# Optimization experiments

Measured on AMD Instinct MI355X. Metric: run time of the kernel, lower is better.

The kernel has to match this reference:

```python
import math
import jax, jax.numpy as jnp
import numpy as np

B, T, D = 8, 2048, 1024

def _gelu(x):
    # tanh-approx GELU, matching the torch module's _gelu
    c = math.sqrt(2.0 / math.pi)
    return 0.5 * x * (1.0 + jnp.tanh(c * (x + 0.044715 * x * x * x)))

def _normalize(x, axis):
    # matches F.normalize(eps=1e-12)
    n = jnp.linalg.norm(x, axis=axis, keepdims=True)
    return x / jnp.maximum(n, 1e-12)

def setup_inputs() -> dict:
    key = jax.random.key(0)
    k1, k2 = jax.random.split(key)
    x = jax.random.normal(k1, (B, T, D), dtype=jnp.float32)
    ema_out = _normalize(jax.random.normal(k2, (D,), dtype=jnp.float32), 0)[..., 0] if False else None
    ema = jax.random.normal(k2, (D,), dtype=jnp.float32)
    ema = ema / jnp.maximum(jnp.linalg.norm(ema), 1e-12)
    return {
        "x": x,
        "ema_out": ema,
        "logit_decay": jnp.float32(math.log(0.9 / 0.1)),
        "log_tau": jnp.float32(math.log(2.0)),
        "log_blend": jnp.float32(math.log(0.3 / 0.7)),
        "logit_blend_seq": jnp.float32(0.0),
    }

def reference(x, ema_out, logit_decay, log_tau, log_blend, logit_blend_seq):
    Bx, Tx, Dx = x.shape
    tau = jnp.exp(log_tau)
    alpha = jax.nn.sigmoid(log_blend)
    w_seq = jax.nn.sigmoid(logit_blend_seq)

    out = _gelu(x)                              # [B,T,D]
    out_norm = _normalize(out, -1)              # [B,T,D]
    ema_norm = ema_out / jnp.maximum(jnp.linalg.norm(ema_out), 1e-12)  # [D]

    ema_sim = jnp.einsum('btd,d->bt', out_norm, ema_norm)             # [B,T]
    sim_mat = jnp.einsum('btd,bsd->bts', out_norm, out_norm)          # [B,T,T]

    causal = jnp.tril(jnp.ones((Tx, Tx), dtype=bool), k=-1)           # strict past
    sim_past = jnp.where(causal[None], sim_mat, -2.0)
    seq_sim = jnp.max(sim_past, axis=-1)                              # [B,T]

    has_past = (jnp.arange(Tx) > 0)[None, :]                          # [1,T]
    seq_sim = jnp.where(has_past, seq_sim, ema_sim)

    familiarity = w_seq * seq_sim + (1.0 - w_seq) * ema_sim
    novelty = jnp.exp(-tau * familiarity)
    gate = 1.0 - alpha + alpha * novelty                              # [B,T]
    return out * gate[..., None]
```

## Files before the change

### kernel.cpp

```cpp
#include <hip/hip_runtime.h>
#include <math.h>

#define NB 8
#define TT 2048
#define DD 1024
#define NTI 16
#define NPAIR 136

typedef __attribute__((ext_vector_type(4))) int intx4;
typedef __attribute__((ext_vector_type(4))) float floatx4;

__device__ inline float fast_gelu(float x) {
    float z = 0.7978845608028654f * (x + 0.044715f * x * x * x);
    float e = __expf(2.0f * z);
    float th = 1.0f - 2.0f / (e + 1.0f);
    return 0.5f * x * (1.0f + th);
}

__global__ __launch_bounds__(256) void k_gelu_norm(
        const float* __restrict__ x, const float* __restrict__ ema,
        unsigned int* __restrict__ onrm8, float* __restrict__ ema_sim) {
    int row = blockIdx.x * 4 + (threadIdx.x >> 6);
    int lane = threadIdx.x & 63;
    const float4* xr = reinterpret_cast<const float4*>(x + (size_t)row * DD);
    const float4* er = reinterpret_cast<const float4*>(ema);
    float g[16];
    float ss = 0.f, dt = 0.f, e2 = 0.f;
#pragma unroll
    for (int j = 0; j < 4; ++j) {
        float4 v = xr[j * 64 + lane];
        float4 e = er[j * 64 + lane];
        float vv[4] = {v.x, v.y, v.z, v.w};
        float ee[4] = {e.x, e.y, e.z, e.w};
        e2 += ee[0] * ee[0] + ee[1] * ee[1] + ee[2] * ee[2] + ee[3] * ee[3];
#pragma unroll
        for (int i = 0; i < 4; ++i) {
            float o = fast_gelu(vv[i]);
            g[j * 4 + i] = o;
            ss += o * o;
            dt += o * ee[i];
        }
    }
#pragma unroll
    for (int m = 1; m < 64; m <<= 1) {
        ss += __shfl_xor(ss, m);
        dt += __shfl_xor(dt, m);
        e2 += __shfl_xor(e2, m);
    }
    float inv = 1.0f / fmaxf(sqrtf(ss), 1e-12f);
    float einv = 1.0f / fmaxf(sqrtf(e2), 1e-12f);
    unsigned int* o8 = onrm8 + (size_t)row * (DD / 4);
#pragma unroll
    for (int j = 0; j < 4; ++j) {
        int q0 = (int)rintf(g[j * 4 + 0] * inv * 127.0f);
        int q1 = (int)rintf(g[j * 4 + 1] * inv * 127.0f);
        int q2 = (int)rintf(g[j * 4 + 2] * inv * 127.0f);
        int q3 = (int)rintf(g[j * 4 + 3] * inv * 127.0f);
        unsigned pk = (q0 & 255) | ((q1 & 255) << 8) | ((q2 & 255) << 16) |
                      ((unsigned)(q3 & 255) << 24);
        o8[j * 64 + lane] = pk;
    }
    if (lane == 0) ema_sim[row] = dt * inv * einv;
}

__global__ __launch_bounds__(256) void k_seqmax(const unsigned char* __restrict__ onrm8,
                                                float* __restrict__ part) {
    __shared__ __align__(16) unsigned char lds[32768];

    int id = blockIdx.x;
    int nid = (id & 7) * NPAIR + (id >> 3);
    int b = nid / NPAIR;
    int p = nid % NPAIR;
    int ti = (int)((sqrtf(8.0f * (float)p + 1.0f) - 1.0f) * 0.5f);
    while ((ti + 1) * (ti + 2) / 2 <= p) ++ti;
    while (ti * (ti + 1) / 2 > p) --ti;
    int sj = p - ti * (ti + 1) / 2;

    int lane = threadIdx.x & 63;
    int wave = threadIdx.x >> 6;
    int wr = wave >> 1, wc = wave & 1;
    int rl = lane & 15, g = lane >> 4;

    const unsigned char* Abase = onrm8 + (size_t)(b * TT + ti * 128) * DD;
    const unsigned char* Bbase = onrm8 + (size_t)(b * TT + sj * 128) * DD;

    intx4 acc[4][4];
#pragma unroll
    for (int i = 0; i < 4; i++)
#pragma unroll
        for (int j = 0; j < 4; j++) acc[i][j] = (intx4){0, 0, 0, 0};

    auto stage = [&](int kt) {
#pragma unroll
        for (int i = 0; i < 4; ++i) {
            int c = wave * 4 + i;
            int off = c * 1024 + lane * 16;
            int row = off >> 7;
            int colb = (off & 127) ^ ((row & 7) << 4);
            const unsigned char* srcA = Abase + (size_t)row * DD + kt * 128 + colb;
            const unsigned char* srcB = Bbase + (size_t)row * DD + kt * 128 + colb;
            __builtin_amdgcn_global_load_lds(
                (const __attribute__((address_space(1))) unsigned int*)srcA,
                (__attribute__((address_space(3))) unsigned int*)(&lds[0] + c * 1024),
                16, 0, 0);
            __builtin_amdgcn_global_load_lds(
                (const __attribute__((address_space(1))) unsigned int*)srcB,
                (__attribute__((address_space(3))) unsigned int*)(&lds[16384] + c * 1024),
                16, 0, 0);
        }
    };

    auto ldfrag = [&](const unsigned char* base, int r, int ks) -> intx4 {
        int sw = (r & 7) << 4;
        return *(const intx4*)(base + r * 128 + ((ks * 64 + g * 16) ^ sw));
    };

    for (int kt = 0; kt < 8; ++kt) {
        stage(kt);
        __syncthreads();
#pragma unroll
        for (int ks = 0; ks < 2; ++ks) {
            intx4 af[4], bg[4];
#pragma unroll
            for (int f = 0; f < 4; ++f) {
                af[f] = ldfrag(&lds[0], wr * 64 + f * 16 + rl, ks);
                bg[f] = ldfrag(&lds[16384], wc * 64 + f * 16 + rl, ks);
            }
#pragma unroll
            for (int fi = 0; fi < 4; ++fi)
#pragma unroll
                for (int fj = 0; fj < 4; ++fj)
                    acc[fi][fj] = __builtin_amdgcn_mfma_i32_16x16x64_i8(
                        af[fi], bg[fj], acc[fi][fj], 0, 0, 0);
        }
        __syncthreads();
    }

    const float qs = 1.0f / 16129.0f;
    int t0g = ti * 128 + wr * 64;
    int s0g = sj * 128 + wc * 64;
#pragma unroll
    for (int fi = 0; fi < 4; ++fi) {
#pragma unroll
        for (int r = 0; r < 4; ++r) {
            int trow = t0g + fi * 16 + g * 4 + r;
            float m = -2.0f;
#pragma unroll
            for (int fj = 0; fj < 4; ++fj) {
                int scol = s0g + fj * 16 + rl;
                float v = (float)acc[fi][fj][r] * qs;
                m = fmaxf(m, (scol < trow) ? v : -2.0f);
            }
#pragma unroll
            for (int msk = 1; msk < 16; msk <<= 1) m = fmaxf(m, __shfl_xor(m, msk));
            if (rl == 0)
                part[(((size_t)b * 32 + sj * 2 + wc) << 11) + trow] = m;
        }
    }
}

__global__ __launch_bounds__(256) void k_gate(
        const float* __restrict__ x, float* __restrict__ out,
        const float* __restrict__ ema_sim, const float* __restrict__ part,
        const float* __restrict__ log_tau,
        const float* __restrict__ log_blend,
        const float* __restrict__ logit_blend_seq) {
    int row = blockIdx.x * 4 + (threadIdx.x >> 6);
    int lane = threadIdx.x & 63;
    int b = row >> 11;
    int t = row & (TT - 1);

    int n = 2 * ((t >> 7) + 1);
    float m = (lane < n) ? part[(((size_t)b * 32 + lane) << 11) + t] : -2.0f;
#pragma unroll
    for (int msk = 1; msk < 64; msk <<= 1) m = fmaxf(m, __shfl_xor(m, msk));

    float tau = __expf(log_tau[0]);
    float alpha = 1.f / (1.f + __expf(-log_blend[0]));
    float wseq = 1.f / (1.f + __expf(-logit_blend_seq[0]));
    float es = ema_sim[row];
    float sq = (t > 0) ? m : es;
    float fam = wseq * sq + (1.f - wseq) * es;
    float gate = 1.f - alpha + alpha * __expf(-tau * fam);

    const float4* xr = reinterpret_cast<const float4*>(x + (size_t)row * DD);
    float4* orow = reinterpret_cast<float4*>(out + (size_t)row * DD);
#pragma unroll
    for (int j = 0; j < 4; ++j) {
        float4 v = xr[j * 64 + lane];
        float4 o;
        o.x = fast_gelu(v.x) * gate;
        o.y = fast_gelu(v.y) * gate;
        o.z = fast_gelu(v.z) * gate;
        o.w = fast_gelu(v.w) * gate;
        orow[j * 64 + lane] = o;
    }
}

extern "C" void kernel_launch(void* const* d_in, const int* in_sizes, int n_in,
                              void* d_out, int out_size, void* d_ws, size_t ws_size,
                              hipStream_t stream) {
    const float* x = (const float*)d_in[0];
    const float* ema = (const float*)d_in[1];
    const float* log_tau = (const float*)d_in[3];
    const float* log_blend = (const float*)d_in[4];
    const float* logit_bs = (const float*)d_in[5];
    float* out = (float*)d_out;

    char* ws = (char*)d_ws;
    float* ema_sim = (float*)(ws + (4 << 10));
    float* part = (float*)(ws + (132 << 10));
    unsigned char* onrm8 = (unsigned char*)(ws + ((size_t)2304 << 10));

    k_gelu_norm<<<NB * TT / 4, 256, 0, stream>>>(x, ema, (unsigned int*)onrm8, ema_sim);
    k_seqmax<<<NB * NPAIR, 256, 0, stream>>>(onrm8, part);
    k_gate<<<NB * TT / 4, 256, 0, stream>>>(x, out, ema_sim, part,
                                            log_tau, log_blend, logit_bs);
}
```

Baseline: 73.32 us.

## Double-buffer LDS tiles in int8 seqmax GEMM with half-width K steps

Splits the k_seqmax LDS staging into two 16KB buffers with K-tiles of 64 bytes instead of 128. The next tile's global-to-LDS loads are issued before computing on the current one, with explicit vmcnt waits, raw barriers and raised wave priority around the MFMA block. The aim is to overlap global memory latency with MFMA work instead of stalling after each stage. In exchange it doubles the iteration count and barrier count, and it relies on hand-placed waitcnt values that must match the number of outstanding loads.

Result: no change. 72.88 us (median of 2 runs) (-0.6%).

```diff
diff --git a/kernel.cpp b/kernel.cpp
--- a/kernel.cpp
+++ b/kernel.cpp
@@ -65,7 +65,7 @@
 
 __global__ __launch_bounds__(256) void k_seqmax(const unsigned char* __restrict__ onrm8,
                                                 float* __restrict__ part) {
-    __shared__ __align__(16) unsigned char lds[32768];
+    __shared__ __align__(16) unsigned char lds[2][16384];
 
     int id = blockIdx.x;
     int nid = (id & 7) * NPAIR + (id >> 3);
@@ -90,50 +90,59 @@
 #pragma unroll
         for (int j = 0; j < 4; j++) acc[i][j] = (intx4){0, 0, 0, 0};
 
-    auto stage = [&](int kt) {
-#pragma unroll
-        for (int i = 0; i < 4; ++i) {
-            int c = wave * 4 + i;
+    auto stage = [&](int buf, int kt) {
+#pragma unroll
+        for (int i = 0; i < 2; ++i) {
+            int c = wave * 2 + i;
             int off = c * 1024 + lane * 16;
-            int row = off >> 7;
-            int colb = (off & 127) ^ ((row & 7) << 4);
-            const unsigned char* srcA = Abase + (size_t)row * DD + kt * 128 + colb;
-            const unsigned char* srcB = Bbase + (size_t)row * DD + kt * 128 + colb;
+            int row = off >> 6;
+            int colb = (off & 63) ^ (((row >> 1) & 3) << 4);
+            const unsigned char* srcA = Abase + (size_t)row * DD + kt * 64 + colb;
+            const unsigned char* srcB = Bbase + (size_t)row * DD + kt * 64 + colb;
             __builtin_amdgcn_global_load_lds(
                 (const __attribute__((address_space(1))) unsigned int*)srcA,
-                (__attribute__((address_space(3))) unsigned int*)(&lds[0] + c * 1024),
+                (__attribute__((address_space(3))) unsigned int*)(&lds[buf][0] + c * 1024),
                 16, 0, 0);
             __builtin_amdgcn_global_load_lds(
                 (const __attribute__((address_space(1))) unsigned int*)srcB,
-                (__attribute__((address_space(3))) unsigned int*)(&lds[16384] + c * 1024),
+                (__attribute__((address_space(3))) unsigned int*)(&lds[buf][8192] + c * 1024),
                 16, 0, 0);
         }
     };
 
-    auto ldfrag = [&](const unsigned char* base, int r, int ks) -> intx4 {
-        int sw = (r & 7) << 4;
-        return *(const intx4*)(base + r * 128 + ((ks * 64 + g * 16) ^ sw));
+    auto ldfrag = [&](const unsigned char* base, int r) -> intx4 {
+        return *(const intx4*)(base + r * 64 + ((g * 16) ^ (((r >> 1) & 3) << 4)));
     };
 
-    for (int kt = 0; kt < 8; ++kt) {
-        stage(kt);
-        __syncthreads();
-#pragma unroll
-        for (int ks = 0; ks < 2; ++ks) {
-            intx4 af[4], bg[4];
-#pragma unroll
-            for (int f = 0; f < 4; ++f) {
-                af[f] = ldfrag(&lds[0], wr * 64 + f * 16 + rl, ks);
-                bg[f] = ldfrag(&lds[16384], wc * 64 + f * 16 + rl, ks);
-            }
-#pragma unroll
-            for (int fi = 0; fi < 4; ++fi)
-#pragma unroll
-                for (int fj = 0; fj < 4; ++fj)
-                    acc[fi][fj] = __builtin_amdgcn_mfma_i32_16x16x64_i8(
-                        af[fi], bg[fj], acc[fi][fj], 0, 0, 0);
-        }
-        __syncthreads();
+    stage(0, 0);
+    for (int kt = 0; kt < 16; ++kt) {
+        int buf = kt & 1;
+        if (kt + 1 < 16) {
+            stage(buf ^ 1, kt + 1);
+            asm volatile("s_waitcnt vmcnt(4)" ::: "memory");
+        } else {
+            asm volatile("s_waitcnt vmcnt(0)" ::: "memory");
+        }
+        __builtin_amdgcn_s_barrier();
+        __builtin_amdgcn_sched_barrier(0);
+        const unsigned char* Ab = &lds[buf][0];
+        const unsigned char* Bb = &lds[buf][8192];
+        intx4 af[4], bg[4];
+#pragma unroll
+        for (int f = 0; f < 4; ++f) {
+            af[f] = ldfrag(Ab, wr * 64 + f * 16 + rl);
+            bg[f] = ldfrag(Bb, wc * 64 + f * 16 + rl);
+        }
+        __builtin_amdgcn_s_setprio(1);
+#pragma unroll
+        for (int fi = 0; fi < 4; ++fi)
+#pragma unroll
+            for (int fj = 0; fj < 4; ++fj)
+                acc[fi][fj] = __builtin_amdgcn_mfma_i32_16x16x64_i8(
+                    af[fi], bg[fj], acc[fi][fj], 0, 0, 0);
+        __builtin_amdgcn_s_setprio(0);
+        __builtin_amdgcn_sched_barrier(0);
+        __builtin_amdgcn_s_barrier();
     }
 
     const float qs = 1.0f / 16129.0f;
```
